# Kernel tuning notes

Measured on AMD Instinct MI355X. Metric: run time of the kernel, lower is better.

The kernel has to match this reference:

```python
import jax, jax.numpy as jnp
import numpy as np

B, D, L, E, R = 16384, 512, 3, 4, 128

def setup_inputs() -> dict:
    key = jax.random.key(0)
    ks = jax.random.split(key, 6)
    scale = 0.05  # keep tanh in its non-saturated regime, like glorot-ish init
    return {
        "x":  jax.random.normal(ks[0], (B, D), dtype=jnp.float32),
        "Us": jax.random.normal(ks[1], (L, E, D, R), dtype=jnp.float32) * scale,
        "Cs": jax.random.normal(ks[2], (L, E, R, R), dtype=jnp.float32) * scale,
        "Vs": jax.random.normal(ks[3], (L, E, D, R), dtype=jnp.float32) * scale,
        "G":  jax.random.normal(ks[4], (L, E, D), dtype=jnp.float32) * scale,
        "b":  jnp.zeros((L, D), dtype=jnp.float32),
    }

def reference(x, Us, Cs, Vs, G, b):
    # x: (B, D). Original keeps x as (B, D, 1); we drop the trailing singleton.
    x0 = x
    xl = x
    num_layers = Us.shape[0]
    for i in range(num_layers):  # small fixed layer count
        U, C, V, g, bias = Us[i], Cs[i], Vs[i], G[i], b[i]
        # per-expert low-rank bilinear transform, fused over experts via einsum
        xv = jnp.tanh(jnp.einsum('edr,bd->ber', V, xl))       # (B, E, R)
        xc = jnp.tanh(jnp.einsum('ers,bes->ber', C, xv))      # (B, E, R)
        xu = jnp.einsum('edr,ber->bed', U, xc)                # (B, E, D)
        cross = x0[:, None, :] * (xu + bias[None, None, :])   # (B, E, D) experts
        # gating: Dense(1, no bias) per expert -> scores (B, E, 1)
        scores = jnp.einsum('bd,ed->be', xl, g)[..., None]
        # NOTE: original applies softmax over the LAST axis of (B, E, 1),
        # a singleton axis, so gates are all ones. Reproduced faithfully.
        gate = jax.nn.softmax(scores, axis=-1)                # (B, E, 1) of ones
        moe = jnp.einsum('bed,be->bd', cross, gate[..., 0])   # (B, D)
        xl = moe + xl
    return xl
```

## Files before the change

### kernel.cpp

```cpp
#include <hip/hip_runtime.h>
#include <hip/hip_bf16.h>

#define BATCH  16384
#define DIM    512
#define NLAYER 3
#define NEXP   4
#define RANK   128

typedef __bf16 bf16_t;
typedef bf16_t bf16x8 __attribute__((ext_vector_type(8)));
typedef bf16_t bf16x4 __attribute__((ext_vector_type(4)));
typedef float  f32x4  __attribute__((ext_vector_type(4)));

__device__ __forceinline__ float tanh_fast(float x) {
    float e = __expf(2.0f * x);
    return 1.0f - 2.0f * __builtin_amdgcn_rcpf(e + 1.0f);
}
__device__ __forceinline__ int swz(int row, int b) { return b ^ ((row & 7) << 4); }

__device__ __forceinline__ bf16x8 ldsr(const bf16_t* base, int row, int kb) {
    return *(const bf16x8*)((const char*)base + row * 1024 + swz(row, kb));
}
__device__ __forceinline__ void ldsw2(bf16_t* base, int row, int cb, bf16_t v) {
    *(bf16_t*)((char*)base + row * 1024 + swz(row, cb)) = v;
}
__device__ __forceinline__ void barrier_lds() {
    asm volatile("s_waitcnt lgkmcnt(0)" ::: "memory");
    __builtin_amdgcn_s_barrier();
}

__global__ void prep_pack(const float* __restrict__ Vs,
                          const float* __restrict__ Us,
                          const float* __restrict__ Cs,
                          bf16_t* __restrict__ Vp,
                          bf16_t* __restrict__ Up,
                          bf16_t* __restrict__ Cp) {
    int t = blockIdx.x * 256 + threadIdx.x;
    if (t < 98304) {
        int lane = t & 63, ni = (t >> 6) & 3, ks = (t >> 8) & 15,
            wn = (t >> 12) & 7, l = t >> 15;
        int c = wn * 64 + ni * 16 + (lane & 15), e = c >> 7, r = c & 127;
        int d0 = ks * 32 + (lane >> 4) * 8;
        const float* src = Vs + ((size_t)(l * NEXP + e) * DIM + d0) * RANK + r;
        bf16x8 v;
        #pragma unroll
        for (int j = 0; j < 8; ++j) v[j] = (bf16_t)src[j * RANK];
        *(bf16x8*)(Vp + (size_t)t * 8) = v;
    } else if (t < 196608) {
        int q = t - 98304;
        int lane = q & 63, ni = (q >> 6) & 3, ks = (q >> 8) & 15,
            wn = (q >> 12) & 7, l = q >> 15;
        int d = wn * 64 + ni * 16 + (lane & 15);
        int k0 = ks * 32 + (lane >> 4) * 8, e = k0 >> 7, r0 = k0 & 127;
        const float* src = Us + ((size_t)(l * NEXP + e) * DIM + d) * RANK + r0;
        bf16x8 v;
        #pragma unroll
        for (int j = 0; j < 8; ++j) v[j] = (bf16_t)src[j];
        *(bf16x8*)(Up + (size_t)q * 8) = v;
    } else if (t < 221184) {
        int q = t - 196608;
        int lane = q & 63, ni = (q >> 6) & 3, k4 = (q >> 8) & 3,
            wn = (q >> 10) & 7, l = q >> 13;
        int e = wn >> 1, rp = (wn & 1) * 64 + ni * 16 + (lane & 15);
        int s0 = k4 * 32 + (lane >> 4) * 8;
        const float* src = Cs + ((size_t)(l * NEXP + e) * RANK + rp) * RANK + s0;
        bf16x8 v;
        #pragma unroll
        for (int j = 0; j < 8; ++j) v[j] = (bf16_t)src[j];
        *(bf16x8*)(Cp + (size_t)q * 8) = v;
    }
}


__global__ __launch_bounds__(512)
void k_layer(const float* xl_in,
             const float* __restrict__ x0,
             const bf16_t* __restrict__ Vw0,
             const bf16_t* __restrict__ Uw0,
             const bf16_t* __restrict__ Cw0,
             const float* __restrict__ bl,
             float* xl_out)
{
    __shared__ __align__(16) char smem[65536];
    bf16_t* bufA = (bf16_t*)smem;
    bf16_t* bufB = (bf16_t*)(smem + 32768);

    const int tid  = threadIdx.x;
    const int lane = tid & 63;
    const int wn   = tid >> 6;
    const int lr   = lane & 15;
    const int lg   = lane >> 4;
    const int m0   = blockIdx.x * 32;

    #pragma unroll
    for (int it = 0; it < 8; ++it) {
        int q = tid + 512 * it;
        int row = q >> 7, c4 = (q & 127) << 2;
        float4 v = *(const float4*)(xl_in + (size_t)(m0 + row) * DIM + c4);
        bf16x4 b4 = { (bf16_t)v.x, (bf16_t)v.y, (bf16_t)v.z, (bf16_t)v.w };
        *(bf16x4*)((char*)bufA + row * 1024 + swz(row, c4 * 2)) = b4;
    }
    barrier_lds();

    const bf16_t* Vw = Vw0 + ((size_t)wn << 15) + lane * 8;
    const bf16_t* Uw = Uw0 + ((size_t)wn << 15) + lane * 8;
    const bf16_t* Cw = Cw0 + ((size_t)wn << 13) + lane * 8;

    {
        f32x4 a1[2][4] = {};
        const bf16_t* vp = Vw;
        #pragma unroll 4
        for (int ks = 0; ks < 16; ++ks) {
            bf16x8 bv[4];
            #pragma unroll
            for (int ni = 0; ni < 4; ++ni)
                bv[ni] = *(const bf16x8*)(vp + ni * 512);
            vp += 2048;
            #pragma unroll
            for (int mi = 0; mi < 2; ++mi) {
                bf16x8 av = ldsr(bufA, mi * 16 + lr, ks * 64 + lg * 16);
                #pragma unroll
                for (int ni = 0; ni < 4; ++ni)
                    a1[mi][ni] = __builtin_amdgcn_mfma_f32_16x16x32_bf16(
                        av, bv[ni], a1[mi][ni], 0, 0, 0);
            }
        }
        #pragma unroll
        for (int mi = 0; mi < 2; ++mi)
            #pragma unroll
            for (int ni = 0; ni < 4; ++ni)
                #pragma unroll
                for (int j = 0; j < 4; ++j)
                    ldsw2(bufB, mi * 16 + lg * 4 + j,
                          (wn * 64 + ni * 16 + lr) * 2,
                          (bf16_t)tanh_fast(a1[mi][ni][j]));
        barrier_lds();
    }

    {
        const int eb = (wn >> 1) * 256;
        f32x4 a2[2][4] = {};
        #pragma unroll
        for (int k4 = 0; k4 < 4; ++k4) {
            bf16x8 bv[4];
            #pragma unroll
            for (int ni = 0; ni < 4; ++ni)
                bv[ni] = *(const bf16x8*)(Cw + (k4 * 4 + ni) * 512);
            #pragma unroll
            for (int mi = 0; mi < 2; ++mi) {
                bf16x8 av = ldsr(bufB, mi * 16 + lr, eb + k4 * 64 + lg * 16);
                #pragma unroll
                for (int ni = 0; ni < 4; ++ni)
                    a2[mi][ni] = __builtin_amdgcn_mfma_f32_16x16x32_bf16(
                        av, bv[ni], a2[mi][ni], 0, 0, 0);
            }
        }
        #pragma unroll
        for (int mi = 0; mi < 2; ++mi)
            #pragma unroll
            for (int ni = 0; ni < 4; ++ni)
                #pragma unroll
                for (int j = 0; j < 4; ++j)
                    ldsw2(bufA, mi * 16 + lg * 4 + j,
                          (wn * 64 + ni * 16 + lr) * 2,
                          (bf16_t)tanh_fast(a2[mi][ni][j]));
        barrier_lds();
    }

    {
        f32x4 a3[2][4] = {};
        const bf16_t* up = Uw;
        #pragma unroll 4
        for (int ks = 0; ks < 16; ++ks) {
            bf16x8 bv[4];
            #pragma unroll
            for (int ni = 0; ni < 4; ++ni)
                bv[ni] = *(const bf16x8*)(up + ni * 512);
            up += 2048;
            #pragma unroll
            for (int mi = 0; mi < 2; ++mi) {
                bf16x8 av = ldsr(bufA, mi * 16 + lr, ks * 64 + lg * 16);
                #pragma unroll
                for (int ni = 0; ni < 4; ++ni)
                    a3[mi][ni] = __builtin_amdgcn_mfma_f32_16x16x32_bf16(
                        av, bv[ni], a3[mi][ni], 0, 0, 0);
            }
        }

        #pragma unroll
        for (int ni = 0; ni < 4; ++ni) {
            int col = wn * 64 + ni * 16 + lr;
            float b4v = 4.0f * bl[col];
            #pragma unroll
            for (int mi = 0; mi < 2; ++mi)
                #pragma unroll
                for (int j = 0; j < 4; ++j) {
                    size_t idx = (size_t)(m0 + mi * 16 + lg * 4 + j) * DIM + col;
                    xl_out[idx] = xl_in[idx] + x0[idx] * (a3[mi][ni][j] + b4v);
                }
        }
    }
}


extern "C" void kernel_launch(void* const* d_in, const int* in_sizes, int n_in,
                              void* d_out, int out_size, void* d_ws, size_t ws_size,
                              hipStream_t stream) {
    const float* x  = (const float*)d_in[0];
    const float* Us = (const float*)d_in[1];
    const float* Cs = (const float*)d_in[2];
    const float* Vs = (const float*)d_in[3];
    const float* bb = (const float*)d_in[5];
    float* out = (float*)d_out;

    bf16_t* Vp = (bf16_t*)d_ws;
    bf16_t* Up = Vp + 786432;
    bf16_t* Cp = Up + 786432;

    prep_pack<<<864, 256, 0, stream>>>(Vs, Us, Cs, Vp, Up, Cp);

    for (int l = 0; l < NLAYER; ++l) {
        k_layer<<<BATCH / 32, 512, 0, stream>>>(
            (l == 0) ? x : out,
            x,
            Vp + (size_t)l * 262144,
            Up + (size_t)l * 262144,
            Cp + (size_t)l * 65536,
            bb + (size_t)l * DIM,
            out);
    }
}
```

Measured before the change: 139.9 us.

## Double M tile to 64 rows and stream weights via async global-to-LDS double buffer

Each block now handles 64 batch rows instead of 32, halving the number of blocks and doubling reuse of every weight fragment loaded. The V and U weight slices are staged into LDS with global_load_lds in a double-buffered pipeline that prefetches the next k-slice during the current MFMAs. Activations share a single 64 KB buffer, so extra barriers are added before the in-place tanh writes. This raises LDS use to 128 KB per block and doubles accumulator registers, which limits occupancy to one block per CU and leaves only 256 blocks in the grid.

```diff
diff --git a/kernel.cpp b/kernel.cpp
--- a/kernel.cpp
+++ b/kernel.cpp
@@ -27,6 +27,11 @@
 __device__ __forceinline__ void barrier_lds() {
     asm volatile("s_waitcnt lgkmcnt(0)" ::: "memory");
     __builtin_amdgcn_s_barrier();
+}
+__device__ __forceinline__ void stage1k(const bf16_t* g, bf16_t* l) {
+    __builtin_amdgcn_global_load_lds(
+        (const __attribute__((address_space(1))) void*)g,
+        (__attribute__((address_space(3))) void*)l, 16, 0, 0);
 }
 
 __global__ void prep_pack(const float* __restrict__ Vs,
@@ -81,65 +86,82 @@
              const float* __restrict__ bl,
              float* xl_out)
 {
-    __shared__ __align__(16) char smem[65536];
-    bf16_t* bufA = (bf16_t*)smem;
-    bf16_t* bufB = (bf16_t*)(smem + 32768);
+    __shared__ __align__(16) char smem[131072];
+    bf16_t* act = (bf16_t*)smem;
+    bf16_t* wsl = (bf16_t*)(smem + 65536);
 
     const int tid  = threadIdx.x;
     const int lane = tid & 63;
     const int wn   = tid >> 6;
     const int lr   = lane & 15;
     const int lg   = lane >> 4;
-    const int m0   = blockIdx.x * 32;
+    const int m0   = blockIdx.x * 64;
 
     #pragma unroll
-    for (int it = 0; it < 8; ++it) {
+    for (int it = 0; it < 16; ++it) {
         int q = tid + 512 * it;
         int row = q >> 7, c4 = (q & 127) << 2;
         float4 v = *(const float4*)(xl_in + (size_t)(m0 + row) * DIM + c4);
         bf16x4 b4 = { (bf16_t)v.x, (bf16_t)v.y, (bf16_t)v.z, (bf16_t)v.w };
-        *(bf16x4*)((char*)bufA + row * 1024 + swz(row, c4 * 2)) = b4;
+        *(bf16x4*)((char*)act + row * 1024 + swz(row, c4 * 2)) = b4;
     }
     barrier_lds();
 
     const bf16_t* Vw = Vw0 + ((size_t)wn << 15) + lane * 8;
     const bf16_t* Uw = Uw0 + ((size_t)wn << 15) + lane * 8;
     const bf16_t* Cw = Cw0 + ((size_t)wn << 13) + lane * 8;
+    bf16_t* ws = wsl + wn * 4096;
 
     {
-        f32x4 a1[2][4] = {};
-        const bf16_t* vp = Vw;
-        #pragma unroll 4
+        asm volatile("s_waitcnt vmcnt(0)" ::: "memory");
+        #pragma unroll
+        for (int c = 0; c < 4; ++c)
+            stage1k(Vw + c * 512, ws + c * 512);
+        f32x4 acc[4][4] = {};
+        #pragma unroll
         for (int ks = 0; ks < 16; ++ks) {
+            const int p = ks & 1;
+            if (ks < 15) {
+                const bf16_t* src = Vw + (ks + 1) * 2048;
+                bf16_t* dst = ws + (p ^ 1) * 2048;
+                #pragma unroll
+                for (int c = 0; c < 4; ++c)
+                    stage1k(src + c * 512, dst + c * 512);
+                asm volatile("s_waitcnt vmcnt(4)" ::: "memory");
+            } else {
+                asm volatile("s_waitcnt vmcnt(0)" ::: "memory");
+            }
+            __builtin_amdgcn_sched_barrier(0);
             bf16x8 bv[4];
             #pragma unroll
             for (int ni = 0; ni < 4; ++ni)
-                bv[ni] = *(const bf16x8*)(vp + ni * 512);
-            vp += 2048;
-            #pragma unroll
-            for (int mi = 0; mi < 2; ++mi) {
-                bf16x8 av = ldsr(bufA, mi * 16 + lr, ks * 64 + lg * 16);
+                bv[ni] = *(const bf16x8*)(ws + p * 2048 + ni * 512 + lane * 8);
+            #pragma unroll
+            for (int mi = 0; mi < 4; ++mi) {
+                bf16x8 av = ldsr(act, mi * 16 + lr, ks * 64 + lg * 16);
                 #pragma unroll
                 for (int ni = 0; ni < 4; ++ni)
-                    a1[mi][ni] = __builtin_amdgcn_mfma_f32_16x16x32_bf16(
-                        av, bv[ni], a1[mi][ni], 0, 0, 0);
-            }
-        }
-        #pragma unroll
-        for (int mi = 0; mi < 2; ++mi)
+                    acc[mi][ni] = __builtin_amdgcn_mfma_f32_16x16x32_bf16(
+                        av, bv[ni], acc[mi][ni], 0, 0, 0);
+            }
+        }
+        __builtin_amdgcn_sched_barrier(0);
+        barrier_lds();
+        #pragma unroll
+        for (int mi = 0; mi < 4; ++mi)
             #pragma unroll
             for (int ni = 0; ni < 4; ++ni)
                 #pragma unroll
                 for (int j = 0; j < 4; ++j)
-                    ldsw2(bufB, mi * 16 + lg * 4 + j,
+                    ldsw2(act, mi * 16 + lg * 4 + j,
                           (wn * 64 + ni * 16 + lr) * 2,
-                          (bf16_t)tanh_fast(a1[mi][ni][j]));
+                          (bf16_t)tanh_fast(acc[mi][ni][j]));
         barrier_lds();
     }
 
     {
         const int eb = (wn >> 1) * 256;
-        f32x4 a2[2][4] = {};
+        f32x4 a2[4][4] = {};
         #pragma unroll
         for (int k4 = 0; k4 < 4; ++k4) {
             bf16x8 bv[4];
@@ -147,39 +169,54 @@
             for (int ni = 0; ni < 4; ++ni)
                 bv[ni] = *(const bf16x8*)(Cw + (k4 * 4 + ni) * 512);
             #pragma unroll
-            for (int mi = 0; mi < 2; ++mi) {
-                bf16x8 av = ldsr(bufB, mi * 16 + lr, eb + k4 * 64 + lg * 16);
+            for (int mi = 0; mi < 4; ++mi) {
+                bf16x8 av = ldsr(act, mi * 16 + lr, eb + k4 * 64 + lg * 16);
                 #pragma unroll
                 for (int ni = 0; ni < 4; ++ni)
                     a2[mi][ni] = __builtin_amdgcn_mfma_f32_16x16x32_bf16(
                         av, bv[ni], a2[mi][ni], 0, 0, 0);
             }
         }
-        #pragma unroll
-        for (int mi = 0; mi < 2; ++mi)
+        barrier_lds();
+        #pragma unroll
+        for (int mi = 0; mi < 4; ++mi)
             #pragma unroll
             for (int ni = 0; ni < 4; ++ni)
                 #pragma unroll
                 for (int j = 0; j < 4; ++j)
-                    ldsw2(bufA, mi * 16 + lg * 4 + j,
+                    ldsw2(act, mi * 16 + lg * 4 + j,
                           (wn * 64 + ni * 16 + lr) * 2,
                           (bf16_t)tanh_fast(a2[mi][ni][j]));
         barrier_lds();
     }
 
     {
-        f32x4 a3[2][4] = {};
-        const bf16_t* up = Uw;
-        #pragma unroll 4
+        asm volatile("s_waitcnt vmcnt(0)" ::: "memory");
+        #pragma unroll
+        for (int c = 0; c < 4; ++c)
+            stage1k(Uw + c * 512, ws + c * 512);
+        f32x4 a3[4][4] = {};
+        #pragma unroll
         for (int ks = 0; ks < 16; ++ks) {
+            const int p = ks & 1;
+            if (ks < 15) {
+                const bf16_t* src = Uw + (ks + 1) * 2048;
+                bf16_t* dst = ws + (p ^ 1) * 2048;
+                #pragma unroll
+                for (int c = 0; c < 4; ++c)
+                    stage1k(src + c * 512, dst + c * 512);
+                asm volatile("s_waitcnt vmcnt(4)" ::: "memory");
+            } else {
+                asm volatile("s_waitcnt vmcnt(0)" ::: "memory");
+            }
+            __builtin_amdgcn_sched_barrier(0);
             bf16x8 bv[4];
             #pragma unroll
             for (int ni = 0; ni < 4; ++ni)
-                bv[ni] = *(const bf16x8*)(up + ni * 512);
-            up += 2048;
-            #pragma unroll
-            for (int mi = 0; mi < 2; ++mi) {
-                bf16x8 av = ldsr(bufA, mi * 16 + lr, ks * 64 + lg * 16);
+                bv[ni] = *(const bf16x8*)(ws + p * 2048 + ni * 512 + lane * 8);
+            #pragma unroll
+            for (int mi = 0; mi < 4; ++mi) {
+                bf16x8 av = ldsr(act, mi * 16 + lr, ks * 64 + lg * 16);
                 #pragma unroll
                 for (int ni = 0; ni < 4; ++ni)
                     a3[mi][ni] = __builtin_amdgcn_mfma_f32_16x16x32_bf16(
@@ -192,7 +229,7 @@
             int col = wn * 64 + ni * 16 + lr;
             float b4v = 4.0f * bl[col];
             #pragma unroll
-            for (int mi = 0; mi < 2; ++mi)
+            for (int mi = 0; mi < 4; ++mi)
                 #pragma unroll
                 for (int j = 0; j < 4; ++j) {
                     size_t idx = (size_t)(m0 + mi * 16 + lg * 4 + j) * DIM + col;
@@ -220,7 +257,7 @@
     prep_pack<<<864, 256, 0, stream>>>(Vs, Us, Cs, Vp, Up, Cp);
 
     for (int l = 0; l < NLAYER; ++l) {
-        k_layer<<<BATCH / 32, 512, 0, stream>>>(
+        k_layer<<<BATCH / 64, 512, 0, stream>>>(
             (l == 0) ? x : out,
             x,
             Vp + (size_t)l * 262144,
```

Result: faster. 133.9 us (-4.3%).
